# Kernel optimization log

Hardware: AMD Instinct MI355X
Metric: run time of the kernel (lower is better)

The kernel has to match this reference:

```python
import jax, jax.numpy as jnp
import numpy as np

N_NODES = 100000
N_EDGES = 1600000
IN_DIM = 128
OUT_DIM = 64
HEADS = 4
NEG_SLOPE = 0.2  # PyG GATConv default
LN_EPS = 1e-5


def setup_inputs() -> dict:
    key = jax.random.key(0)
    ks = jax.random.split(key, 8)
    x = jax.random.normal(ks[0], (N_NODES, IN_DIM), dtype=jnp.float32)
    edge_index = jax.random.randint(ks[1], (2, N_EDGES), 0, N_NODES, dtype=jnp.int64)
    # GATConv params: lin weight, per-head attention vectors, output bias (concat=False)
    s = 1.0 / np.sqrt(IN_DIM)
    W = jax.random.uniform(ks[2], (IN_DIM, HEADS * OUT_DIM), jnp.float32, -s, s)
    att_src = jax.random.uniform(ks[3], (HEADS, OUT_DIM), jnp.float32, -s, s)
    att_dst = jax.random.uniform(ks[4], (HEADS, OUT_DIM), jnp.float32, -s, s)
    bias = jnp.zeros((OUT_DIM,), jnp.float32)
    gamma = jnp.ones((OUT_DIM,), jnp.float32)
    beta = jnp.zeros((OUT_DIM,), jnp.float32)
    return {"x": x, "edge_index": edge_index, "W": W, "att_src": att_src,
            "att_dst": att_dst, "bias": bias, "gamma": gamma, "beta": beta}


def reference(x, edge_index, W, att_src, att_dst, bias, gamma, beta):
    N = x.shape[0]
    H, C = att_src.shape
    # Linear projection, split heads: (N, H, C)
    xl = (x @ W).reshape(N, H, C)
    # Per-node attention logits: (N, H)
    a_src = jnp.einsum('nhc,hc->nh', xl, att_src)
    a_dst = jnp.einsum('nhc,hc->nh', xl, att_dst)
    # Add self-loops (PyG GATConv default add_self_loops=True)
    loops = jnp.arange(N, dtype=edge_index.dtype)
    src = jnp.concatenate([edge_index[0], loops])  # (E+N,)
    dst = jnp.concatenate([edge_index[1], loops])
    # Per-edge attention: gather, leaky_relu, segment softmax over destination
    alpha = jax.nn.leaky_relu(a_src[src] + a_dst[dst], NEG_SLOPE)  # (E+N, H)
    amax = jax.ops.segment_max(alpha, dst, num_segments=N)  # (N, H)
    e = jnp.exp(alpha - amax[dst])
    denom = jax.ops.segment_sum(e, dst, num_segments=N)  # (N, H)
    alpha = e / (denom[dst] + 1e-16)
    # Message passing: scatter-add alpha-weighted source features to dst
    msg = xl[src] * alpha[:, :, None]  # (E+N, H, C)
    out = jax.ops.segment_sum(msg, dst, num_segments=N)  # (N, H, C)
    out = out.mean(axis=1) + bias  # concat=False -> head average, (N, C)
    # LayerNorm
    mu = out.mean(axis=-1, keepdims=True)
    var = out.var(axis=-1, keepdims=True)
    return (out - mu) * jax.lax.rsqrt(var + LN_EPS) * gamma + beta
```

## Files before the change

kernel.cpp:

```cpp
#include <hip/hip_runtime.h>
#include <hip/hip_fp16.h>

#define IN_DIM   128
#define HC       256
#define OUT_DIM  64
#define HEADS    4
#define NEG_SLOPE 0.2f
#define LN_EPS   1e-5f
#define DBITS    5
#define DPB      32
#define MAXBINS  4096
#define CAP      768
#define NHIST    256
#define SCAT_TPE 16

typedef short bf16x8 __attribute__((ext_vector_type(8)));
typedef float f32x4  __attribute__((ext_vector_type(4)));

__device__ __forceinline__ float lrelu(float a){ return a > 0.f ? a : NEG_SLOPE * a; }

__device__ __forceinline__ unsigned short f2bf(float f){
  unsigned u = __float_as_uint(f);
  u = u + 0x7fffu + ((u >> 16) & 1u);
  return (unsigned short)(u >> 16);
}
__device__ __forceinline__ unsigned pk2(float a, float b){
  return (unsigned)f2bf(a) | ((unsigned)f2bf(b) << 16);
}
__device__ __forceinline__ __half2 u2h(unsigned u){ return *(__half2*)&u; }
__device__ __forceinline__ unsigned h2u(__half2 h){ return *(unsigned*)&h; }

__device__ __forceinline__ bool detect32(const int* ei){
  int ln = threadIdx.x & 63;
  unsigned probe = (ln < 32) ? (unsigned)ei[2*ln + 1] : 0u;
  return __ballot(probe != 0) != 0ull;
}

__global__ __launch_bounds__(256) void k_front(
    const float* __restrict__ W, unsigned short* __restrict__ Wt,
    const int* ei, int* __restrict__ bincnt, int E, int nbins)
{
  if (blockIdx.x < 128){
    int n = blockIdx.x*2 + (threadIdx.x >> 7);
    int k = threadIdx.x & 127;
    Wt[n*IN_DIM + k] = f2bf(W[k*HC + n]);
    return;
  }
  __shared__ int h[MAXBINS];
  bool i32 = detect32(ei);
  for (int i = threadIdx.x; i < nbins; i += 256) h[i] = 0;
  __syncthreads();
  int slot = blockIdx.x - 128;
  if (i32){
    const int* dstp = ei + E;
    for (int e = slot*256 + threadIdx.x; e < E; e += NHIST*256)
      atomicAdd(&h[dstp[e] >> DBITS], 1);
  } else {
    const long long* dstp = (const long long*)ei + E;
    for (int e = slot*256 + threadIdx.x; e < E; e += NHIST*256)
      atomicAdd(&h[((int)dstp[e]) >> DBITS], 1);
  }
  __syncthreads();
  for (int i = threadIdx.x; i < nbins; i += 256)
    if (h[i]) atomicAdd(&bincnt[i], h[i]);
}

__global__ __launch_bounds__(1024) void k_binscan(const int* __restrict__ bincnt,
    int* binstart, int* bincur, int nbins, int E)
{
  __shared__ int sh[1024];
  int t = threadIdx.x;
  int v[4]; int s = 0;
  #pragma unroll
  for (int k = 0; k < 4; ++k){
    int i = 4*t + k;
    v[k] = (i < nbins) ? bincnt[i] : 0;
    s += v[k];
  }
  sh[t] = s; __syncthreads();
  #pragma unroll
  for (int off = 1; off < 1024; off <<= 1){
    int u = (t >= off) ? sh[t-off] : 0;
    __syncthreads();
    sh[t] += u;
    __syncthreads();
  }
  int run = sh[t] - s;
  #pragma unroll
  for (int k = 0; k < 4; ++k){
    int i = 4*t + k;
    if (i < nbins){ binstart[i] = run; bincur[i] = run; }
    run += v[k];
  }
  if (t == 0) binstart[nbins] = E;
}

__device__ __forceinline__ void gemm_body(int bid, char* smem,
    const float* __restrict__ x, const unsigned short* __restrict__ Wt,
    const float* __restrict__ att_s, const float* __restrict__ att_d,
    __half* __restrict__ xl_t, float* __restrict__ a_src,
    float* __restrict__ a_dst, int N)
{
  unsigned short* sxl = (unsigned short*)(smem + 16384);
  int t = threadIdx.x;
  int nb = bid * 64;

  #pragma unroll
  for (int it = 0; it < 4; ++it){
    int idx = it*256 + t;
    int row = idx >> 4, seg = idx & 15;
    uint4 pk = make_uint4(0,0,0,0);
    if (nb + row < N){
      const float* xr = x + (size_t)(nb + row)*IN_DIM + seg*8;
      float4 f0 = *(const float4*)xr;
      float4 f1 = *(const float4*)(xr + 4);
      pk.x = pk2(f0.x, f0.y); pk.y = pk2(f0.z, f0.w);
      pk.z = pk2(f1.x, f1.y); pk.w = pk2(f1.z, f1.w);
    }
    int byte = (row*256 + seg*16) ^ ((row & 7) << 4);
    *(uint4*)(smem + byte) = pk;
  }
  __syncthreads();

  int w = t >> 6, l = t & 63;

  bf16x8 bfr[4][4];
  #pragma unroll
  for (int nt = 0; nt < 4; ++nt){
    int col = w*64 + nt*16 + (l & 15);
    #pragma unroll
    for (int ks = 0; ks < 4; ++ks)
      bfr[nt][ks] = *(const bf16x8*)(Wt + (size_t)col*IN_DIM + ks*32 + ((l >> 4) << 3));
  }
  float attS[4], attD[4];
  #pragma unroll
  for (int nt = 0; nt < 4; ++nt){
    attS[nt] = att_s[w*64 + nt*16 + (l & 15)];
    attD[nt] = att_d[w*64 + nt*16 + (l & 15)];
  }

  #pragma unroll
  for (int sub = 0; sub < 4; ++sub){
    bf16x8 afr[4];
    #pragma unroll
    for (int ks = 0; ks < 4; ++ks){
      int row = sub*16 + (l & 15);
      int byte = (row*256 + ks*64 + ((l >> 4) << 4)) ^ ((row & 7) << 4);
      afr[ks] = *(const bf16x8*)(smem + byte);
    }
    f32x4 acc[4] = {{0,0,0,0},{0,0,0,0},{0,0,0,0},{0,0,0,0}};
    #pragma unroll
    for (int nt = 0; nt < 4; ++nt)
      #pragma unroll
      for (int ks = 0; ks < 4; ++ks)
        acc[nt] = __builtin_amdgcn_mfma_f32_16x16x32_bf16(afr[ks], bfr[nt][ks], acc[nt], 0, 0, 0);

    #pragma unroll
    for (int r = 0; r < 4; ++r){
      float ps = 0.f, pd = 0.f;
      #pragma unroll
      for (int nt = 0; nt < 4; ++nt){
        ps = fmaf(acc[nt][r], attS[nt], ps);
        pd = fmaf(acc[nt][r], attD[nt], pd);
      }
      #pragma unroll
      for (int o = 8; o; o >>= 1){ ps += __shfl_xor(ps, o); pd += __shfl_xor(pd, o); }
      int node = nb + sub*16 + (l >> 4)*4 + r;
      if ((l & 15) == 0 && node < N){
        a_src[node*4 + w] = ps;
        a_dst[node*4 + w] = pd;
      }
    }

    #pragma unroll
    for (int nt = 0; nt < 4; ++nt){
      int ch = nt*16 + (l & 15);
      #pragma unroll
      for (int r = 0; r < 4; ++r){
        int row = (l >> 4)*4 + r;
        sxl[row*HC + ch*4 + w] = __half_as_ushort(__float2half(acc[nt][r]));
      }
    }
    __syncthreads();
    const uint4* s4 = (const uint4*)sxl;
    uint4* g4 = (uint4*)(xl_t + (size_t)(nb + sub*16)*HC);
    #pragma unroll
    for (int c = t; c < 512; c += 256){
      int row = c >> 5;
      if (nb + sub*16 + row < N) g4[c] = s4[c];
    }
    __syncthreads();
  }
}

__device__ __forceinline__ void scat_body(int bid, char* smem,
    const int* ei, int* bincur, unsigned* tmp, int E, int nbins)
{
  int* h32  = (int*)smem;
  int* base = (int*)(smem + 8192);
  bool i32 = detect32(ei);
  int tile0 = bid * (256*SCAT_TPE);
  for (int i = threadIdx.x; i < ((nbins+1)>>1); i += 256) h32[i] = 0;
  __syncthreads();
  unsigned pk[SCAT_TPE]; int rk[SCAT_TPE];
  #pragma unroll
  for (int k = 0; k < SCAT_TPE; ++k){
    int e = tile0 + k*256 + threadIdx.x;
    if (e < E){
      int s, d;
      if (i32){ s = ei[e]; d = ei[E + e]; }
      else {
        s = (int)((const long long*)ei)[e];
        d = (int)((const long long*)ei)[(size_t)E + e];
      }
      int b = d >> DBITS;
      pk[k] = (unsigned)s | ((unsigned)(d & (DPB-1)) << 20);
      int sh = (b & 1) << 4;
      unsigned old = (unsigned)atomicAdd(&h32[b >> 1], 1 << sh);
      rk[k] = (int)((old >> sh) & 0xFFFFu) | (b << 12);
    }
  }
  __syncthreads();
  for (int i = threadIdx.x; i < nbins; i += 256){
    int c = (h32[i >> 1] >> ((i & 1) << 4)) & 0xFFFF;
    base[i] = c ? atomicAdd(&bincur[i], c) : 0;
  }
  __syncthreads();
  #pragma unroll
  for (int k = 0; k < SCAT_TPE; ++k){
    int e = tile0 + k*256 + threadIdx.x;
    if (e < E){
      int b = rk[k] >> 12, r = rk[k] & 0xFFF;
      tmp[base[b] + r] = pk[k];
    }
  }
}

__global__ __launch_bounds__(256) void k_gemm_scat(
    const float* __restrict__ x, const unsigned short* __restrict__ Wt,
    const float* __restrict__ att_s, const float* __restrict__ att_d,
    __half* __restrict__ xl_t, float* __restrict__ a_src, float* __restrict__ a_dst,
    int N, const int* ei, int* bincur, unsigned* tmp, int E, int nbins,
    int gemmBlocks)
{
  __shared__ char smem[24576];
  int bid = (int)blockIdx.x;
  if (bid < gemmBlocks)
    gemm_body(bid, smem, x, Wt, att_s, att_d, xl_t, a_src, a_dst, N);
  else
    scat_body(bid - gemmBlocks, smem, ei, bincur, tmp, E, nbins);
}

__global__ __launch_bounds__(256) void k_node(
    const int* __restrict__ binstart, const unsigned* __restrict__ tmp,
    int* __restrict__ csr,
    const float4* __restrict__ a_src4, const float4* __restrict__ a_dst4,
    const __half* __restrict__ xl_t,
    const float* __restrict__ bias, const float* __restrict__ gamma,
    const float* __restrict__ beta, float* __restrict__ out, int N)
{
  __shared__ int cnt[DPB], sc[DPB], cur[DPB];
  __shared__ int lcsr[CAP];
  __shared__ uint2 wlds[16][16];
  int b = blockIdx.x, tid = threadIdx.x;
  int s0 = binstart[b], s1 = binstart[b+1];
  int seg = s1 - s0;

  if (tid < DPB){ cnt[tid] = 0; }
  __syncthreads();
  for (int e = s0 + tid; e < s1; e += 256)
    atomicAdd(&cnt[(tmp[e] >> 20) & (DPB-1)], 1);
  __syncthreads();
  if (tid < DPB) sc[tid] = cnt[tid];
  __syncthreads();
  #pragma unroll
  for (int off = 1; off < DPB; off <<= 1){
    int v = (tid < DPB && tid >= off) ? sc[tid-off] : 0;
    __syncthreads();
    if (tid < DPB) sc[tid] += v;
    __syncthreads();
  }
  if (tid < DPB){ int ex = sc[tid] - cnt[tid]; sc[tid] = ex; cur[tid] = ex; }
  __syncthreads();

  int* ebuf = (seg <= CAP) ? lcsr : (csr + s0);
  for (int e = s0 + tid; e < s1; e += 256){
    unsigned u = tmp[e];
    int dl = (u >> 20) & (DPB-1);
    int r = atomicAdd(&cur[dl], 1);
    ebuf[r] = (int)(u & 0xFFFFFu);
  }
  __syncthreads();

  int gg = tid >> 4, i = tid & 15;
  #pragma unroll
  for (int n = 0; n < 2; ++n){
    int dl = gg*2 + n;
    int node = b*DPB + dl;
    if (node >= N) continue;
    int lstart = sc[dl], lend = lstart + cnt[dl];

    float4 ad  = a_dst4[node];
    float4 asl = a_src4[node];
    float es0 = __expf(lrelu(asl.x + ad.x));
    float es1 = __expf(lrelu(asl.y + ad.y));
    float es2 = __expf(lrelu(asl.z + ad.z));
    float es3 = __expf(lrelu(asl.w + ad.w));

    __half2 s01 = __floats2half2_rn(es0, es1);
    __half2 s23 = __floats2half2_rn(es2, es3);
    const uint4* ps = (const uint4*)((const char*)xl_t + ((size_t)node*512 + (i << 5)));
    uint4 xa = ps[0], xb = ps[1];
    __half2 acc[8];
    acc[0] = __hmul2(s01, u2h(xa.x));
    acc[1] = __hmul2(s23, u2h(xa.y));
    acc[2] = __hmul2(s01, u2h(xa.z));
    acc[3] = __hmul2(s23, u2h(xa.w));
    acc[4] = __hmul2(s01, u2h(xb.x));
    acc[5] = __hmul2(s23, u2h(xb.y));
    acc[6] = __hmul2(s01, u2h(xb.z));
    acc[7] = __hmul2(s23, u2h(xb.w));
    float lp0 = 0.f, lp1 = 0.f, lp2 = 0.f, lp3 = 0.f;

    for (int t2 = lstart; t2 < lend; t2 += 16){
      int rem = lend - t2; if (rem > 16) rem = 16;
      float e0 = 0.f, e1 = 0.f, e2 = 0.f, e3 = 0.f;
      if (i < rem){
        int sid = ebuf[t2 + i];
        float4 as4 = a_src4[sid];
        e0 = __expf(lrelu(as4.x + ad.x));
        e1 = __expf(lrelu(as4.y + ad.y));
        e2 = __expf(lrelu(as4.z + ad.z));
        e3 = __expf(lrelu(as4.w + ad.w));
        lp0 += e0; lp1 += e1; lp2 += e2; lp3 += e3;
      }
      wlds[gg][i] = make_uint2(h2u(__floats2half2_rn(e0, e1)),
                               h2u(__floats2half2_rn(e2, e3)));

      #pragma unroll 4
      for (int j = 0; j < rem; ++j){
        uint2 wpk = wlds[gg][j];
        int sj = ebuf[t2 + j];
        __half2 w01 = u2h(wpk.x), w23 = u2h(wpk.y);
        const uint4* p = (const uint4*)((const char*)xl_t + ((size_t)sj*512 + (i << 5)));
        uint4 ya = p[0], yb = p[1];
        acc[0] = __hfma2(w01, u2h(ya.x), acc[0]);
        acc[1] = __hfma2(w23, u2h(ya.y), acc[1]);
        acc[2] = __hfma2(w01, u2h(ya.z), acc[2]);
        acc[3] = __hfma2(w23, u2h(ya.w), acc[3]);
        acc[4] = __hfma2(w01, u2h(yb.x), acc[4]);
        acc[5] = __hfma2(w23, u2h(yb.y), acc[5]);
        acc[6] = __hfma2(w01, u2h(yb.z), acc[6]);
        acc[7] = __hfma2(w23, u2h(yb.w), acc[7]);
      }
    }

    __half2 lp01 = __floats2half2_rn(lp0, lp1);
    __half2 lp23 = __floats2half2_rn(lp2, lp3);
    #pragma unroll
    for (int o = 8; o; o >>= 1){
      lp01 = __hadd2(lp01, u2h(__shfl_xor(h2u(lp01), o)));
      lp23 = __hadd2(lp23, u2h(__shfl_xor(h2u(lp23), o)));
    }
    float r0 = __builtin_amdgcn_rcpf(__low2float(lp01) + es0);
    float r1 = __builtin_amdgcn_rcpf(__high2float(lp01) + es1);
    float r2 = __builtin_amdgcn_rcpf(__low2float(lp23) + es2);
    float r3 = __builtin_amdgcn_rcpf(__high2float(lp23) + es3);

    float4 b4 = *(const float4*)(bias + 4*i);
    float o0 = 0.25f*(__low2float(acc[0])*r0 + __high2float(acc[0])*r1 +
                      __low2float(acc[1])*r2 + __high2float(acc[1])*r3) + b4.x;
    float o1 = 0.25f*(__low2float(acc[2])*r0 + __high2float(acc[2])*r1 +
                      __low2float(acc[3])*r2 + __high2float(acc[3])*r3) + b4.y;
    float o2 = 0.25f*(__low2float(acc[4])*r0 + __high2float(acc[4])*r1 +
                      __low2float(acc[5])*r2 + __high2float(acc[5])*r3) + b4.z;
    float o3 = 0.25f*(__low2float(acc[6])*r0 + __high2float(acc[6])*r1 +
                      __low2float(acc[7])*r2 + __high2float(acc[7])*r3) + b4.w;

    float s  = o0 + o1 + o2 + o3;
    float sq = o0*o0 + o1*o1 + o2*o2 + o3*o3;
    #pragma unroll
    for (int o = 8; o; o >>= 1){
      s  += __shfl_xor(s, o);
      sq += __shfl_xor(sq, o);
    }
    float mu = s * (1.f/OUT_DIM);
    float var = sq * (1.f/OUT_DIM) - mu*mu;
    float rs = rsqrtf(var + LN_EPS);
    float4 g4v = *(const float4*)(gamma + 4*i);
    float4 be4 = *(const float4*)(beta + 4*i);
    float4 ov;
    ov.x = (o0 - mu)*rs*g4v.x + be4.x;
    ov.y = (o1 - mu)*rs*g4v.y + be4.y;
    ov.z = (o2 - mu)*rs*g4v.z + be4.z;
    ov.w = (o3 - mu)*rs*g4v.w + be4.w;
    *(float4*)(out + (size_t)node*OUT_DIM + 4*i) = ov;
  }
}

extern "C" void kernel_launch(void* const* d_in, const int* in_sizes, int n_in,
                              void* d_out, int out_size, void* d_ws, size_t ws_size,
                              hipStream_t stream)
{
  const float* x     = (const float*)d_in[0];
  const int*   ei    = (const int*)d_in[1];
  const float* W     = (const float*)d_in[2];
  const float* att_s = (const float*)d_in[3];
  const float* att_d = (const float*)d_in[4];
  const float* bias  = (const float*)d_in[5];
  const float* gamma = (const float*)d_in[6];
  const float* beta  = (const float*)d_in[7];
  float* out = (float*)d_out;

  int N = in_sizes[0] / IN_DIM;
  int E = in_sizes[1] / 2;
  int nbins = (N + DPB - 1) >> DBITS;

  char* ws = (char*)d_ws;
  __half* xl_t = (__half*)ws;                   ws += (size_t)N*HC*sizeof(__half);
  float* a_src = (float*)ws;                    ws += (size_t)N*HEADS*sizeof(float);
  float* a_dst = (float*)ws;                    ws += (size_t)N*HEADS*sizeof(float);
  int* csr      = (int*)ws;                     ws += (size_t)E*sizeof(int);
  unsigned* tmp = (unsigned*)ws;                ws += (size_t)E*sizeof(unsigned);
  int* bincnt   = (int*)ws;                     ws += MAXBINS*sizeof(int);
  int* binstart = (int*)ws;                     ws += (MAXBINS+1)*sizeof(int);
  int* bincur   = (int*)ws;                     ws += MAXBINS*sizeof(int);
  unsigned short* Wt = (unsigned short*)ws;     ws += (size_t)HC*IN_DIM*sizeof(unsigned short);

  int gemmBlocks = (N + 63)/64;
  int scatBlocks = (E + 256*SCAT_TPE - 1)/(256*SCAT_TPE);

  hipMemsetAsync(bincnt, 0, (size_t)nbins*sizeof(int), stream);
  k_front   <<<128 + NHIST, 256, 0, stream>>>(W, Wt, ei, bincnt, E, nbins);
  k_binscan <<<1, 1024, 0, stream>>>(bincnt, binstart, bincur, nbins, E);
  k_gemm_scat<<<gemmBlocks + scatBlocks, 256, 0, stream>>>(
      x, Wt, att_s, att_d, xl_t, a_src, a_dst, N, ei, bincur, tmp, E, nbins,
      gemmBlocks);
  k_node    <<<nbins, 256, 0, stream>>>(binstart, tmp, csr,
              (const float4*)a_src, (const float4*)a_dst, xl_t,
              bias, gamma, beta, out, N);
}
```

Measured before the change: 219.2 us.

## Halve GEMM row tile and use larger two-pass scatter tiles

The GEMM block now handles 32 rows instead of 64, which halves its shared-memory footprint and doubles the GEMM block count. The scatter blocks now cover 16384 edges each and run two passes: the first counts destinations into the per-block histogram, the second re-reads the edges and uses a second round of shared atomics to compute each edge's rank. This removes the per-thread register arrays and cuts the number of per-block global atomics on bincur, at the cost of reading the edge list twice and doing more LDS atomics. Larger tiles also mean each block's writes into a bin are more contiguous.

```diff
diff --git a/kernel.cpp b/kernel.cpp
--- a/kernel.cpp
+++ b/kernel.cpp
@@ -12,7 +12,7 @@
 #define MAXBINS  4096
 #define CAP      768
 #define NHIST    256
-#define SCAT_TPE 16
+#define TILE_E   16384
 
 typedef short bf16x8 __attribute__((ext_vector_type(8)));
 typedef float f32x4  __attribute__((ext_vector_type(4)));
@@ -101,12 +101,12 @@
     __half* __restrict__ xl_t, float* __restrict__ a_src,
     float* __restrict__ a_dst, int N)
 {
-  unsigned short* sxl = (unsigned short*)(smem + 16384);
+  unsigned short* sxl = (unsigned short*)(smem + 8192);
   int t = threadIdx.x;
-  int nb = bid * 64;
-
-  #pragma unroll
-  for (int it = 0; it < 4; ++it){
+  int nb = bid * 32;
+
+  #pragma unroll
+  for (int it = 0; it < 2; ++it){
     int idx = it*256 + t;
     int row = idx >> 4, seg = idx & 15;
     uint4 pk = make_uint4(0,0,0,0);
@@ -140,7 +140,7 @@
   }
 
   #pragma unroll
-  for (int sub = 0; sub < 4; ++sub){
+  for (int sub = 0; sub < 2; ++sub){
     bf16x8 afr[4];
     #pragma unroll
     for (int ks = 0; ks < 4; ++ks){
@@ -199,25 +199,22 @@
   int* h32  = (int*)smem;
   int* base = (int*)(smem + 8192);
   bool i32 = detect32(ei);
-  int tile0 = bid * (256*SCAT_TPE);
-  for (int i = threadIdx.x; i < ((nbins+1)>>1); i += 256) h32[i] = 0;
-  __syncthreads();
-  unsigned pk[SCAT_TPE]; int rk[SCAT_TPE];
-  #pragma unroll
-  for (int k = 0; k < SCAT_TPE; ++k){
-    int e = tile0 + k*256 + threadIdx.x;
-    if (e < E){
-      int s, d;
-      if (i32){ s = ei[e]; d = ei[E + e]; }
-      else {
-        s = (int)((const long long*)ei)[e];
-        d = (int)((const long long*)ei)[(size_t)E + e];
-      }
-      int b = d >> DBITS;
-      pk[k] = (unsigned)s | ((unsigned)(d & (DPB-1)) << 20);
-      int sh = (b & 1) << 4;
-      unsigned old = (unsigned)atomicAdd(&h32[b >> 1], 1 << sh);
-      rk[k] = (int)((old >> sh) & 0xFFFFu) | (b << 12);
+  int e0 = bid * TILE_E;
+  int e1 = e0 + TILE_E; if (e1 > E) e1 = E;
+  int nh = (nbins + 1) >> 1;
+  for (int i = threadIdx.x; i < nh; i += 256) h32[i] = 0;
+  __syncthreads();
+  if (i32){
+    const int* dstp = ei + E;
+    for (int e = e0 + threadIdx.x; e < e1; e += 256){
+      int b = dstp[e] >> DBITS;
+      atomicAdd(&h32[b >> 1], 1 << ((b & 1) << 4));
+    }
+  } else {
+    const long long* dstp = (const long long*)ei + E;
+    for (int e = e0 + threadIdx.x; e < e1; e += 256){
+      int b = ((int)dstp[e]) >> DBITS;
+      atomicAdd(&h32[b >> 1], 1 << ((b & 1) << 4));
     }
   }
   __syncthreads();
@@ -226,13 +223,20 @@
     base[i] = c ? atomicAdd(&bincur[i], c) : 0;
   }
   __syncthreads();
-  #pragma unroll
-  for (int k = 0; k < SCAT_TPE; ++k){
-    int e = tile0 + k*256 + threadIdx.x;
-    if (e < E){
-      int b = rk[k] >> 12, r = rk[k] & 0xFFF;
-      tmp[base[b] + r] = pk[k];
-    }
+  for (int i = threadIdx.x; i < nh; i += 256) h32[i] = 0;
+  __syncthreads();
+  for (int e = e0 + threadIdx.x; e < e1; e += 256){
+    int s, d;
+    if (i32){ s = ei[e]; d = ei[E + e]; }
+    else {
+      s = (int)((const long long*)ei)[e];
+      d = (int)((const long long*)ei)[(size_t)E + e];
+    }
+    int b = d >> DBITS;
+    int sh = (b & 1) << 4;
+    unsigned old = (unsigned)atomicAdd(&h32[b >> 1], 1 << sh);
+    int r = (int)((old >> sh) & 0xFFFFu);
+    tmp[base[b] + r] = (unsigned)s | ((unsigned)(d & (DPB-1)) << 20);
   }
 }
 
@@ -427,8 +431,8 @@
   int* bincur   = (int*)ws;                     ws += MAXBINS*sizeof(int);
   unsigned short* Wt = (unsigned short*)ws;     ws += (size_t)HC*IN_DIM*sizeof(unsigned short);
 
-  int gemmBlocks = (N + 63)/64;
-  int scatBlocks = (E + 256*SCAT_TPE - 1)/(256*SCAT_TPE);
+  int gemmBlocks = (N + 31)/32;
+  int scatBlocks = (E + TILE_E - 1)/TILE_E;
 
   hipMemsetAsync(bincnt, 0, (size_t)nbins*sizeof(int), stream);
   k_front   <<<128 + NHIST, 256, 0, stream>>>(W, Wt, ei, bincnt, E, nbins);
```

Result: slower. 248.7 us (+13.5%).
